# Optimization experiments

Hardware: AMD Instinct MI355X
Metric: run time of the kernel (lower is better)

The kernel has to match this reference:

```python
import jax, jax.numpy as jnp
import numpy as np

MAX_SHIFT = 2
SMOOTH = 1.0

def setup_inputs() -> dict:
    key = jax.random.key(0)
    k1, k2 = jax.random.split(key)
    # predicted probabilities in [0,1)
    inputs = jax.random.uniform(k1, (64, 1, 512, 512), dtype=jnp.float32)
    # soft targets (the original accepts any float mask); uniform works as a stand-in
    targets = jax.random.uniform(k2, (64, 1, 512, 512), dtype=jnp.float32)
    return {"inputs": inputs, "targets": targets}

def reference(inputs, targets):
    # all (shift_y, shift_x) pairs from the 5x5 nested loop
    shifts = jnp.array(
        [(sy, sx)
         for sx in range(-MAX_SHIFT, MAX_SHIFT + 1)
         for sy in range(-MAX_SHIFT, MAX_SHIFT + 1)],
        dtype=jnp.int32,
    )  # [25, 2]

    # global sums; targets.sum() is invariant under roll but kept per the original math
    i_sum = inputs.sum()
    t_sum = targets.sum()

    def dice_loss(shift):
        st = jnp.roll(targets, (shift[0], shift[1]), axis=(2, 3))
        intersection = jnp.sum(inputs * st)
        return 1.0 - (2.0 * intersection + SMOOTH) / (i_sum + t_sum + SMOOTH)

    losses = jax.vmap(dice_loss)(shifts)  # [25]
    return jnp.min(losses)
```

## Files before the change

kernel.cpp:

```cpp
#include <hip/hip_runtime.h>

#define H 512
#define W 512

__device__ __forceinline__ float wave_sum_dpp(float x) {
#define DPP_STEP(ctrl)                                                          \
    x += __int_as_float(__builtin_amdgcn_update_dpp(                            \
        0, __float_as_int(x), (ctrl), 0xF, 0xF, true))
    DPP_STEP(0x111);
    DPP_STEP(0x112);
    DPP_STEP(0x114);
    DPP_STEP(0x118);
    DPP_STEP(0x142);
    DPP_STEP(0x143);
#undef DPP_STEP
    return x;
}

__device__ __forceinline__ float4 ld4(const float* p) {
    return *reinterpret_cast<const float4*>(p);
}

__global__ __launch_bounds__(256, 4)
void dice_partial(const float* __restrict__ in, const float* __restrict__ tg,
                  float* __restrict__ ws, int nblocks) {
    __shared__ float warr[4][32];

    const int tid  = threadIdx.x;
    const int wave = tid >> 6, lane = tid & 63;

    const int bid = blockIdx.x;
    const int wrk = (bid & 7) * (nblocks >> 3) + (bid >> 3);

    const int q  = wrk * 4 + wave;
    const int b  = q >> 7;
    const int y0 = (q & 127) << 2;
    const float* __restrict__ ib = in + (size_t)b * (H * W);
    const float* __restrict__ tb = tg + (size_t)b * (H * W);

    const int c0 = lane * 8;
    const int cL = (c0 - 4) & (W - 1);
    const int cR = (c0 + 8) & (W - 1);

    float4 ia[4], ic[4];
#pragma unroll
    for (int yi = 0; yi < 4; ++yi) {
        const float* rp = ib + (size_t)(y0 + yi) * W;
        ia[yi] = ld4(rp + c0);
        ic[yi] = ld4(rp + c0 + 4);
    }

    float4 pa[3], pc[3], pl[3], pr[3];
#define TROW(t) (tb + (size_t)((y0 - 2 + (t)) & (H - 1)) * W)
#define ISSUE(slot, t) {                                        \
        const float* tp = TROW(t);                              \
        pa[slot] = ld4(tp + c0);                                \
        pc[slot] = ld4(tp + c0 + 4);                            \
        pl[slot] = ld4(tp + cL);                                \
        pr[slot] = ld4(tp + cR); }

    ISSUE(0, 0)
    ISSUE(1, 1)

    float iv[4][8];
    float isum = 0.f;
#pragma unroll
    for (int yi = 0; yi < 4; ++yi) {
        iv[yi][0] = ia[yi].x; iv[yi][1] = ia[yi].y;
        iv[yi][2] = ia[yi].z; iv[yi][3] = ia[yi].w;
        iv[yi][4] = ic[yi].x; iv[yi][5] = ic[yi].y;
        iv[yi][6] = ic[yi].z; iv[yi][7] = ic[yi].w;
#pragma unroll
        for (int j = 0; j < 8; ++j) isum += iv[yi][j];
    }

    float acc[25];
#pragma unroll
    for (int k = 0; k < 25; ++k) acc[k] = 0.f;
    float tsum = 0.f;

#pragma unroll
    for (int t = 0; t < 8; ++t) {
        if (t + 2 < 8) { ISSUE((t + 2) % 3, t + 2) }

        const int s = t % 3;
        float tw[12];
        tw[0]  = pl[s].z; tw[1]  = pl[s].w;
        tw[2]  = pa[s].x; tw[3]  = pa[s].y; tw[4] = pa[s].z; tw[5] = pa[s].w;
        tw[6]  = pc[s].x; tw[7]  = pc[s].y; tw[8] = pc[s].z; tw[9] = pc[s].w;
        tw[10] = pr[s].x; tw[11] = pr[s].y;

        if (t >= 2 && t <= 5) {
#pragma unroll
            for (int j = 0; j < 8; ++j) tsum += tw[j + 2];
        }

#pragma unroll
        for (int yi = 0; yi < 4; ++yi) {
            const int sy = yi + 2 - t;
            if (sy < -2 || sy > 2) continue;
#pragma unroll
            for (int sx = -2; sx <= 2; ++sx) {
#pragma unroll
                for (int j = 0; j < 8; ++j)
                    acc[(sy + 2) * 5 + (sx + 2)] += iv[yi][j] * tw[j + 2 - sx];
            }
        }
    }
#undef ISSUE
#undef TROW

#pragma unroll
    for (int k = 0; k < 25; ++k) {
        const float v = wave_sum_dpp(acc[k]);
        if (lane == 63) warr[wave][k] = v;
    }
    {
        const float v = wave_sum_dpp(isum);
        if (lane == 63) warr[wave][25] = v;
        const float u = wave_sum_dpp(tsum);
        if (lane == 63) warr[wave][26] = u;
    }

    __syncthreads();
    if (tid < 27) {
        const float s = warr[0][tid] + warr[1][tid] + warr[2][tid] + warr[3][tid];
        ws[tid * nblocks + bid] = s;
    }
}

__global__ __launch_bounds__(256)
void dice_reduce(const float* __restrict__ ws, float* __restrict__ tot, int nblocks) {
    __shared__ float red[4];
    const int k = blockIdx.x;
    const int tid = threadIdx.x;
    const float* p = ws + (size_t)k * nblocks;

    float s = 0.f;
    for (int i = tid; i < nblocks; i += 256) s += p[i];
    s = wave_sum_dpp(s);
    if ((tid & 63) == 63) red[tid >> 6] = s;
    __syncthreads();
    if (tid == 0) tot[k] = red[0] + red[1] + red[2] + red[3];
}

__global__ void dice_out(const float* __restrict__ tot, float* __restrict__ out) {
    const int tid = threadIdx.x;
    float v = (tid < 25) ? tot[tid] : -1e30f;
#pragma unroll
    for (int off = 32; off; off >>= 1) v = fmaxf(v, __shfl_down(v, off, 64));
    if (tid == 0) {
        const float denom = tot[25] + tot[26] + 1.0f;
        out[0] = 1.0f - (2.0f * v + 1.0f) / denom;
    }
}

extern "C" void kernel_launch(void* const* d_in, const int* in_sizes, int n_in,
                              void* d_out, int out_size, void* d_ws, size_t ws_size,
                              hipStream_t stream) {
    const float* inputs  = (const float*)d_in[0];
    const float* targets = (const float*)d_in[1];
    float* out = (float*)d_out;
    float* ws  = (float*)d_ws;

    const int B = in_sizes[0] / (H * W);
    const int nblocks = B * (H / 4) / 4;

    float* tot = ws + (size_t)27 * nblocks;

    dice_partial<<<nblocks, 256, 0, stream>>>(inputs, targets, ws, nblocks);
    dice_reduce<<<27, 256, 0, stream>>>(ws, tot, nblocks);
    dice_out<<<1, 64, 0, stream>>>(tot, out);
}
```

Measured before the change: 40.22 us.

## Stage target row tiles in LDS via direct global-to-LDS loads

Each block now handles 32 rows with 8 waves and stages the 36 needed target rows, halo included, into LDS using global_load_lds. Waves read their shifted target windows from LDS instead of each loading its own 8 overlapping rows from global memory. This cuts redundant global target traffic from 8 rows per 4 output rows to about 36 per 32. In exchange it uses about 72KB of LDS per block, adds a block barrier, and limits occupancy.

```diff
diff --git a/kernel.cpp b/kernel.cpp
--- a/kernel.cpp
+++ b/kernel.cpp
@@ -2,6 +2,9 @@
 
 #define H 512
 #define W 512
+#define RROWS 32
+#define TGR  (RROWS + 4)
+#define NCHUNK (TGR * 2)
 
 __device__ __forceinline__ float wave_sum_dpp(float x) {
 #define DPP_STEP(ctrl)                                                          \
@@ -20,11 +23,22 @@
 __device__ __forceinline__ float4 ld4(const float* p) {
     return *reinterpret_cast<const float4*>(p);
 }
+__device__ __forceinline__ float2 ld2(const float* p) {
+    return *reinterpret_cast<const float2*>(p);
+}
 
-__global__ __launch_bounds__(256, 4)
+__device__ __forceinline__ void gl_lds16(const float* g, float* l) {
+    __builtin_amdgcn_global_load_lds(
+        (const __attribute__((address_space(1))) void*)g,
+        (__attribute__((address_space(3))) void*)l,
+        16, 0, 0);
+}
+
+__global__ __launch_bounds__(512, 4)
 void dice_partial(const float* __restrict__ in, const float* __restrict__ tg,
                   float* __restrict__ ws, int nblocks) {
-    __shared__ float warr[4][32];
+    __shared__ __align__(16) float tgs[TGR * W];
+    __shared__ float warr[8][32];
 
     const int tid  = threadIdx.x;
     const int wave = tid >> 6, lane = tid & 63;
@@ -32,35 +46,30 @@
     const int bid = blockIdx.x;
     const int wrk = (bid & 7) * (nblocks >> 3) + (bid >> 3);
 
-    const int q  = wrk * 4 + wave;
-    const int b  = q >> 7;
-    const int y0 = (q & 127) << 2;
+    const int b  = wrk >> 4;
+    const int y0 = (wrk & 15) * RROWS;
     const float* __restrict__ ib = in + (size_t)b * (H * W);
     const float* __restrict__ tb = tg + (size_t)b * (H * W);
 
     const int c0 = lane * 8;
-    const int cL = (c0 - 4) & (W - 1);
-    const int cR = (c0 + 8) & (W - 1);
 
+    const int ry = y0 + wave * 4;
     float4 ia[4], ic[4];
 #pragma unroll
     for (int yi = 0; yi < 4; ++yi) {
-        const float* rp = ib + (size_t)(y0 + yi) * W;
+        const float* rp = ib + (size_t)(ry + yi) * W;
         ia[yi] = ld4(rp + c0);
         ic[yi] = ld4(rp + c0 + 4);
     }
 
-    float4 pa[3], pc[3], pl[3], pr[3];
-#define TROW(t) (tb + (size_t)((y0 - 2 + (t)) & (H - 1)) * W)
-#define ISSUE(slot, t) {                                        \
-        const float* tp = TROW(t);                              \
-        pa[slot] = ld4(tp + c0);                                \
-        pc[slot] = ld4(tp + c0 + 4);                            \
-        pl[slot] = ld4(tp + cL);                                \
-        pr[slot] = ld4(tp + cR); }
-
-    ISSUE(0, 0)
-    ISSUE(1, 1)
+#pragma unroll
+    for (int k = 0; k < 9; ++k) {
+        const int c    = wave * 9 + k;
+        const int rr   = c >> 1;
+        const int half = (c & 1) * 256;
+        const int ra   = (y0 - 2 + rr) & (H - 1);
+        gl_lds16(tb + (size_t)ra * W + half + lane * 4, &tgs[c * 256]);
+    }
 
     float iv[4][8];
     float isum = 0.f;
@@ -73,6 +82,10 @@
 #pragma unroll
         for (int j = 0; j < 8; ++j) isum += iv[yi][j];
     }
+    isum = wave_sum_dpp(isum);
+    if (lane == 63) warr[wave][25] = isum;
+
+    __syncthreads();
 
     float acc[25];
 #pragma unroll
@@ -81,14 +94,16 @@
 
 #pragma unroll
     for (int t = 0; t < 8; ++t) {
-        if (t + 2 < 8) { ISSUE((t + 2) % 3, t + 2) }
-
-        const int s = t % 3;
+        const float* rowp = &tgs[(wave * 4 + t) * W];
         float tw[12];
-        tw[0]  = pl[s].z; tw[1]  = pl[s].w;
-        tw[2]  = pa[s].x; tw[3]  = pa[s].y; tw[4] = pa[s].z; tw[5] = pa[s].w;
-        tw[6]  = pc[s].x; tw[7]  = pc[s].y; tw[8] = pc[s].z; tw[9] = pc[s].w;
-        tw[10] = pr[s].x; tw[11] = pr[s].y;
+        const float4 a  = ld4(rowp + c0);
+        const float4 cc = ld4(rowp + c0 + 4);
+        const float2 lf = ld2(rowp + ((c0 - 2) & (W - 1)));
+        const float2 rg = ld2(rowp + ((c0 + 8) & (W - 1)));
+        tw[0]  = lf.x; tw[1]  = lf.y;
+        tw[2]  = a.x;  tw[3]  = a.y;  tw[4] = a.z;  tw[5] = a.w;
+        tw[6]  = cc.x; tw[7]  = cc.y; tw[8] = cc.z; tw[9] = cc.w;
+        tw[10] = rg.x; tw[11] = rg.y;
 
         if (t >= 2 && t <= 5) {
 #pragma unroll
@@ -107,8 +122,6 @@
             }
         }
     }
-#undef ISSUE
-#undef TROW
 
 #pragma unroll
     for (int k = 0; k < 25; ++k) {
@@ -116,15 +129,15 @@
         if (lane == 63) warr[wave][k] = v;
     }
     {
-        const float v = wave_sum_dpp(isum);
-        if (lane == 63) warr[wave][25] = v;
         const float u = wave_sum_dpp(tsum);
         if (lane == 63) warr[wave][26] = u;
     }
 
     __syncthreads();
     if (tid < 27) {
-        const float s = warr[0][tid] + warr[1][tid] + warr[2][tid] + warr[3][tid];
+        float s = 0.f;
+#pragma unroll
+        for (int w = 0; w < 8; ++w) s += warr[w][tid];
         ws[tid * nblocks + bid] = s;
     }
 }
@@ -164,11 +177,11 @@
     float* ws  = (float*)d_ws;
 
     const int B = in_sizes[0] / (H * W);
-    const int nblocks = B * (H / 4) / 4;
+    const int nblocks = B * (H / RROWS);
 
     float* tot = ws + (size_t)27 * nblocks;
 
-    dice_partial<<<nblocks, 256, 0, stream>>>(inputs, targets, ws, nblocks);
+    dice_partial<<<nblocks, 512, 0, stream>>>(inputs, targets, ws, nblocks);
     dice_reduce<<<27, 256, 0, stream>>>(ws, tot, nblocks);
     dice_out<<<1, 64, 0, stream>>>(tot, out);
 }
```

Measured after the change: 38.76 us. 1.04x faster.

## Stage target rows into per-wave LDS ring via direct global-to-LDS loads

Applied to the files above, without the earlier changes.

Target rows are now fetched with global_load_lds into a 4-slot per-wave LDS ring, three rows ahead, with explicit vmcnt waits. Each lane then reads its 12-wide window, including the halo, from LDS. This replaces the four overlapping float4 global loads per row per lane and the register staging they needed. The aim is to cut redundant global/L1 traffic and register pressure while keeping deeper prefetch. The cost is 32KB of LDS per block, which may limit occupancy, plus hand-managed wait counts and an early full wait on the input loads.

```diff
diff --git a/kernel.cpp b/kernel.cpp
--- a/kernel.cpp
+++ b/kernel.cpp
@@ -2,6 +2,8 @@
 
 #define H 512
 #define W 512
+#define NW 4
+#define SLOTS 4
 
 __device__ __forceinline__ float wave_sum_dpp(float x) {
 #define DPP_STEP(ctrl)                                                          \
@@ -20,11 +22,25 @@
 __device__ __forceinline__ float4 ld4(const float* p) {
     return *reinterpret_cast<const float4*>(p);
 }
+__device__ __forceinline__ float2 ld2(const float* p) {
+    return *reinterpret_cast<const float2*>(p);
+}
+
+__device__ __forceinline__ void gl_lds16(const float* g, float* l) {
+    __builtin_amdgcn_global_load_lds(
+        (const __attribute__((address_space(1))) void*)g,
+        (__attribute__((address_space(3))) void*)l,
+        16, 0, 0);
+}
+
+#define WAITV(n) do { asm volatile("s_waitcnt vmcnt(" #n ")" ::: "memory");     \
+                      __builtin_amdgcn_sched_barrier(0); } while (0)
 
 __global__ __launch_bounds__(256, 4)
 void dice_partial(const float* __restrict__ in, const float* __restrict__ tg,
                   float* __restrict__ ws, int nblocks) {
-    __shared__ float warr[4][32];
+    __shared__ __align__(16) float ring[NW][SLOTS][W];
+    __shared__ float warr[NW][32];
 
     const int tid  = threadIdx.x;
     const int wave = tid >> 6, lane = tid & 63;
@@ -35,32 +51,27 @@
     const int q  = wrk * 4 + wave;
     const int b  = q >> 7;
     const int y0 = (q & 127) << 2;
-    const float* __restrict__ ib = in + (size_t)b * (H * W);
-    const float* __restrict__ tb = tg + (size_t)b * (H * W);
+    const float* __restrict__ inb = in + (size_t)b * (H * W);
+    const float* __restrict__ tgb = tg + (size_t)b * (H * W);
 
     const int c0 = lane * 8;
-    const int cL = (c0 - 4) & (W - 1);
-    const int cR = (c0 + 8) & (W - 1);
 
     float4 ia[4], ic[4];
 #pragma unroll
     for (int yi = 0; yi < 4; ++yi) {
-        const float* rp = ib + (size_t)(y0 + yi) * W;
+        const float* rp = inb + (size_t)(y0 + yi) * W;
         ia[yi] = ld4(rp + c0);
         ic[yi] = ld4(rp + c0 + 4);
     }
+    WAITV(0);
 
-    float4 pa[3], pc[3], pl[3], pr[3];
-#define TROW(t) (tb + (size_t)((y0 - 2 + (t)) & (H - 1)) * W)
-#define ISSUE(slot, t) {                                        \
-        const float* tp = TROW(t);                              \
-        pa[slot] = ld4(tp + c0);                                \
-        pc[slot] = ld4(tp + c0 + 4);                            \
-        pl[slot] = ld4(tp + cL);                                \
-        pr[slot] = ld4(tp + cR); }
-
-    ISSUE(0, 0)
-    ISSUE(1, 1)
+#define TISSUE(t, slot) {                                                       \
+        const float* rp = tgb + (size_t)((y0 - 2 + (t)) & (H - 1)) * W;         \
+        gl_lds16(rp + lane * 4,       &ring[wave][slot][0]);                    \
+        gl_lds16(rp + 256 + lane * 4, &ring[wave][slot][256]); }
+    TISSUE(0, 0)
+    TISSUE(1, 1)
+    TISSUE(2, 2)
 
     float iv[4][8];
     float isum = 0.f;
@@ -73,42 +84,52 @@
 #pragma unroll
         for (int j = 0; j < 8; ++j) isum += iv[yi][j];
     }
+    isum = wave_sum_dpp(isum);
+    if (lane == 63) warr[wave][25] = isum;
 
     float acc[25];
 #pragma unroll
     for (int k = 0; k < 25; ++k) acc[k] = 0.f;
     float tsum = 0.f;
 
-#pragma unroll
-    for (int t = 0; t < 8; ++t) {
-        if (t + 2 < 8) { ISSUE((t + 2) % 3, t + 2) }
+#define CONSUME(t) {                                                            \
+        const float* rowp = &ring[wave][(t) & 3][0];                            \
+        float tw[12];                                                           \
+        const float4 a  = ld4(rowp + c0);                                       \
+        const float4 cc = ld4(rowp + c0 + 4);                                   \
+        const float2 lf = ld2(rowp + ((c0 - 2) & (W - 1)));                     \
+        const float2 rg = ld2(rowp + ((c0 + 8) & (W - 1)));                     \
+        tw[0]  = lf.x; tw[1]  = lf.y;                                           \
+        tw[2]  = a.x;  tw[3]  = a.y;  tw[4] = a.z;  tw[5] = a.w;                \
+        tw[6]  = cc.x; tw[7]  = cc.y; tw[8] = cc.z; tw[9] = cc.w;               \
+        tw[10] = rg.x; tw[11] = rg.y;                                           \
+        if ((t) >= 2 && (t) <= 5) {                                             \
+            _Pragma("unroll")                                                   \
+            for (int j = 0; j < 8; ++j) tsum += tw[j + 2];                      \
+        }                                                                       \
+        _Pragma("unroll")                                                       \
+        for (int yi = 0; yi < 4; ++yi) {                                        \
+            const int sy = yi + 2 - (t);                                        \
+            if (sy < -2 || sy > 2) continue;                                    \
+            _Pragma("unroll")                                                   \
+            for (int sx = -2; sx <= 2; ++sx) {                                  \
+                _Pragma("unroll")                                               \
+                for (int j = 0; j < 8; ++j)                                     \
+                    acc[(sy + 2) * 5 + (sx + 2)] += iv[yi][j] * tw[j + 2 - sx]; \
+            }                                                                   \
+        }                                                                       \
+    }
 
-        const int s = t % 3;
-        float tw[12];
-        tw[0]  = pl[s].z; tw[1]  = pl[s].w;
-        tw[2]  = pa[s].x; tw[3]  = pa[s].y; tw[4] = pa[s].z; tw[5] = pa[s].w;
-        tw[6]  = pc[s].x; tw[7]  = pc[s].y; tw[8] = pc[s].z; tw[9] = pc[s].w;
-        tw[10] = pr[s].x; tw[11] = pr[s].y;
-
-        if (t >= 2 && t <= 5) {
-#pragma unroll
-            for (int j = 0; j < 8; ++j) tsum += tw[j + 2];
-        }
-
-#pragma unroll
-        for (int yi = 0; yi < 4; ++yi) {
-            const int sy = yi + 2 - t;
-            if (sy < -2 || sy > 2) continue;
-#pragma unroll
-            for (int sx = -2; sx <= 2; ++sx) {
-#pragma unroll
-                for (int j = 0; j < 8; ++j)
-                    acc[(sy + 2) * 5 + (sx + 2)] += iv[yi][j] * tw[j + 2 - sx];
-            }
-        }
-    }
-#undef ISSUE
-#undef TROW
+    TISSUE(3, 3)  WAITV(6);  CONSUME(0)
+    TISSUE(4, 0)  WAITV(6);  CONSUME(1)
+    TISSUE(5, 1)  WAITV(6);  CONSUME(2)
+    TISSUE(6, 2)  WAITV(6);  CONSUME(3)
+    TISSUE(7, 3)  WAITV(6);  CONSUME(4)
+        WAITV(4);  CONSUME(5)
+                  WAITV(2);  CONSUME(6)
+                  WAITV(0);  CONSUME(7)
+#undef CONSUME
+#undef TISSUE
 
 #pragma unroll
     for (int k = 0; k < 25; ++k) {
@@ -116,8 +137,6 @@
         if (lane == 63) warr[wave][k] = v;
     }
     {
-        const float v = wave_sum_dpp(isum);
-        if (lane == 63) warr[wave][25] = v;
         const float u = wave_sum_dpp(tsum);
         if (lane == 63) warr[wave][26] = u;
     }
```

New measurement: 42.35 us. +5.3%, slower.
